# Optimization experiments

Hardware: AMD Instinct MI355X
Metric: run time of the kernel (lower is better)

The kernel has to match this reference:

```python
import jax, jax.numpy as jnp
import numpy as np

B, L = 131072, 24  # batch size, number of links (= n_dofs, all revolute)


def _skew(v):
    # v: [L, 3] -> [L, 3, 3] cross-product matrices
    zeros = jnp.zeros_like(v[:, 0])
    return jnp.stack([
        jnp.stack([zeros, -v[:, 2], v[:, 1]], axis=-1),
        jnp.stack([v[:, 2], zeros, -v[:, 0]], axis=-1),
        jnp.stack([-v[:, 1], v[:, 0], zeros], axis=-1),
    ], axis=-2)


def setup_inputs() -> dict:
    key = jax.random.key(0)
    k1, k2, k3, k4 = jax.random.split(key, 4)
    q = jax.random.normal(k1, (B, L), dtype=jnp.float32)
    qd = jax.random.normal(k2, (B, L), dtype=jnp.float32)
    axes = jax.random.normal(k3, (L, 3), dtype=jnp.float32)   # joint axes (normalized in reference)
    t_fix = jax.random.normal(k4, (L, 3), dtype=jnp.float32)  # fixed parent->joint translations
    return {"q": q, "qd": qd, "axes": axes, "t_fix": t_fix}


def reference(q, qd, axes, t_fix):
    # Stateless forward kinematics for all links of a serial revolute chain.
    # joint_pose_i = Trans(t_fix_i) @ Rot(axis_i, q_i);  pose_i = pose_{i-1} @ joint_pose_i
    dtype = q.dtype
    a = axes / jnp.linalg.norm(axes, axis=-1, keepdims=True)  # [L,3]
    K = _skew(a)                                              # [L,3,3]
    KK = jnp.einsum('lij,ljk->lik', K, K)
    s = jnp.sin(q)[..., None, None]                           # [B,L,1,1]
    c = jnp.cos(q)[..., None, None]
    I3 = jnp.eye(3, dtype=dtype)
    # Rodrigues: per-joint rotation [B,L,3,3]
    R_joint = I3 + s * K[None] + (1.0 - c) * KK[None]

    def step(carry, x):
        Rp, tp = carry          # parent pose: [B,3,3], [B,3]
        Rj, tf = x              # joint rotation [B,3,3], fixed translation [3]
        tc = tp + jnp.einsum('bij,j->bi', Rp, tf)
        Rc = jnp.einsum('bij,bjk->bik', Rp, Rj)
        return (Rc, tc), (Rc, tc)

    R0 = jnp.broadcast_to(I3, (q.shape[0], 3, 3))
    t0 = jnp.zeros((q.shape[0], 3), dtype=dtype)
    Rj_seq = jnp.moveaxis(R_joint, 1, 0)                      # [L,B,3,3]
    _, (Rs, ts) = jax.lax.scan(step, (R0, t0), (Rj_seq, t_fix))
    Rs = jnp.moveaxis(Rs, 0, 1)                               # [B,L,3,3]
    ts = jnp.moveaxis(ts, 0, 1)                               # [B,L,3]
    top = jnp.concatenate([Rs, ts[..., None]], axis=-1)       # [B,L,3,4]
    bottom = jnp.broadcast_to(jnp.array([0., 0., 0., 1.], dtype=dtype),
                              top.shape[:-2] + (1, 4))
    return jnp.concatenate([top, bottom], axis=-2)            # [B,L,4,4]
```

## Files before the change

### kernel.cpp

```cpp
#include <hip/hip_runtime.h>


typedef float v4 __attribute__((ext_vector_type(4)));

constexpr int L = 24;
constexpr int EW = 384;
constexpr int EWP = 388;
constexpr int WAVE_WORDS = 16 * EWP;

__global__ __launch_bounds__(128) void fk_kernel(
    const float* __restrict__ q,
    const float* __restrict__ axes,
    const float* __restrict__ tfix,
    float* __restrict__ out,
    int nb)
{
    __shared__ float s_a[L * 3];
    __shared__ float s_t[L * 3];
    __shared__ float s_buf[2 * WAVE_WORDS];

    if (threadIdx.x < L) {
        const int l = threadIdx.x;
        float ax = axes[l * 3 + 0], ay = axes[l * 3 + 1], az = axes[l * 3 + 2];
        float inv = rsqrtf(ax * ax + ay * ay + az * az);
        s_a[l * 3 + 0] = ax * inv;
        s_a[l * 3 + 1] = ay * inv;
        s_a[l * 3 + 2] = az * inv;
        s_t[l * 3 + 0] = tfix[l * 3 + 0];
        s_t[l * 3 + 1] = tfix[l * 3 + 1];
        s_t[l * 3 + 2] = tfix[l * 3 + 2];
    }
    __syncthreads();

    const int tid  = threadIdx.x;
    const int wave = tid >> 6;
    const int lane = tid & 63;
    const int e    = lane >> 2;
    const int r    = lane & 3;

    const int wave_elem0 = blockIdx.x * 32 + wave * 16;
    const int b = wave_elem0 + e;

    float* wbuf = s_buf + wave * WAVE_WORDS;

    if (b < nb) {
        float qv[L];
        {
            const v4* q4 = (const v4*)(q + (size_t)b * L);
            #pragma unroll
            for (int i = 0; i < L / 4; ++i) {
                v4 v = q4[i];
                qv[4 * i + 0] = v.x;
                qv[4 * i + 1] = v.y;
                qv[4 * i + 2] = v.z;
                qv[4 * i + 3] = v.w;
            }
        }

        float Ra = (r == 0) ? 1.f : 0.f;
        float Rb = (r == 1) ? 1.f : 0.f;
        float Rc = (r == 2) ? 1.f : 0.f;
        float t  = (r == 3) ? 1.f : 0.f;

        v4* lrow = (v4*)(wbuf + e * EWP + r * 4);

        #pragma unroll
        for (int l = 0; l < L; ++l) {
            const float ax = s_a[l * 3 + 0], ay = s_a[l * 3 + 1], az = s_a[l * 3 + 2];
            const float fx = s_t[l * 3 + 0], fy = s_t[l * 3 + 1], fz = s_t[l * 3 + 2];

            float s, c;
            __sincosf(qv[l], &s, &c);
            const float omc = 1.0f - c;

            const float xy = omc * ax * ay;
            const float xz = omc * ax * az;
            const float yz = omc * ay * az;
            const float J00 = c + omc * ax * ax;
            const float J11 = c + omc * ay * ay;
            const float J22 = c + omc * az * az;
            const float J01 = xy - s * az, J10 = xy + s * az;
            const float J02 = xz + s * ay, J20 = xz - s * ay;
            const float J12 = yz - s * ax, J21 = yz + s * ax;

            t += Ra * fx + Rb * fy + Rc * fz;

            const float na  = Ra * J00 + Rb * J10 + Rc * J20;
            const float nb_ = Ra * J01 + Rb * J11 + Rc * J21;
            const float nc  = Ra * J02 + Rb * J12 + Rc * J22;
            Ra = na; Rb = nb_; Rc = nc;

            lrow[l * 4] = v4{Ra, Rb, Rc, t};
        }
    }
    __syncthreads();

    if (wave_elem0 < nb) {
        float* gbase = out + (size_t)wave_elem0 * EW;
        #pragma unroll
        for (int j = 0; j < 24; ++j) {
            const unsigned w = (unsigned)(j * 256 + lane * 4);
            const unsigned elem = w / EW;
            const unsigned rem  = w - elem * EW;
            v4 v = *(const v4*)(wbuf + elem * EWP + rem);
            __builtin_nontemporal_store(v, (v4*)(gbase + w));
        }
    }
}

extern "C" void kernel_launch(void* const* d_in, const int* in_sizes, int n_in,
                              void* d_out, int out_size, void* d_ws, size_t ws_size,
                              hipStream_t stream) {
    const float* q    = (const float*)d_in[0];
    const float* axes = (const float*)d_in[2];
    const float* tfix = (const float*)d_in[3];
    float* out = (float*)d_out;

    const int nb = in_sizes[0] / L;
    const long long nthreads = (long long)nb * 4;
    const int grid = (int)((nthreads + 127) / 128);
    fk_kernel<<<grid, 128, 0, stream>>>(q, axes, tfix, out, nb);
}
```

Baseline: 222.2 us.

## Store outputs directly from registers, dropping the LDS staging buffer

Removes the per-wave shared-memory staging and the second coalesced, nontemporal write phase. Each thread now writes its 16-byte row straight to global memory, with four adjacent lanes covering 64 contiguous bytes per link. Per-link products of the axis components are precomputed into shared memory and the math is rewritten with explicit FMAs. Blocks grow to 256 threads with a 4-blocks occupancy hint. The risk is that the direct stores are strided across elements, 384 floats apart between lane groups, which may hurt write coalescing compared with the staged, fully contiguous stores.

Result: faster. 214.0 us (-3.7%).

```diff
diff --git a/kernel.cpp b/kernel.cpp
--- a/kernel.cpp
+++ b/kernel.cpp
@@ -4,107 +4,82 @@
 typedef float v4 __attribute__((ext_vector_type(4)));
 
 constexpr int L = 24;
-constexpr int EW = 384;
-constexpr int EWP = 388;
-constexpr int WAVE_WORDS = 16 * EWP;
 
-__global__ __launch_bounds__(128) void fk_kernel(
+__global__ __launch_bounds__(256, 4) void fk_kernel(
     const float* __restrict__ q,
     const float* __restrict__ axes,
     const float* __restrict__ tfix,
     float* __restrict__ out,
     int nb)
 {
-    __shared__ float s_a[L * 3];
-    __shared__ float s_t[L * 3];
-    __shared__ float s_buf[2 * WAVE_WORDS];
+    __shared__ float s_lnk[L][12];
 
     if (threadIdx.x < L) {
         const int l = threadIdx.x;
         float ax = axes[l * 3 + 0], ay = axes[l * 3 + 1], az = axes[l * 3 + 2];
         float inv = rsqrtf(ax * ax + ay * ay + az * az);
-        s_a[l * 3 + 0] = ax * inv;
-        s_a[l * 3 + 1] = ay * inv;
-        s_a[l * 3 + 2] = az * inv;
-        s_t[l * 3 + 0] = tfix[l * 3 + 0];
-        s_t[l * 3 + 1] = tfix[l * 3 + 1];
-        s_t[l * 3 + 2] = tfix[l * 3 + 2];
+        ax *= inv; ay *= inv; az *= inv;
+        s_lnk[l][0] = ax;             s_lnk[l][1] = ay;             s_lnk[l][2] = az;
+        s_lnk[l][3] = tfix[l * 3 + 0]; s_lnk[l][4] = tfix[l * 3 + 1]; s_lnk[l][5] = tfix[l * 3 + 2];
+        s_lnk[l][6] = ax * ax;        s_lnk[l][7] = ay * ay;
+        s_lnk[l][8] = az * az;        s_lnk[l][9] = ax * ay;
+        s_lnk[l][10] = ax * az;       s_lnk[l][11] = ay * az;
     }
     __syncthreads();
 
-    const int tid  = threadIdx.x;
-    const int wave = tid >> 6;
-    const int lane = tid & 63;
-    const int e    = lane >> 2;
-    const int r    = lane & 3;
+    const int tid = blockIdx.x * 256 + threadIdx.x;
+    const int b = tid >> 2;
+    const int r = tid & 3;
+    if (b >= nb) return;
 
-    const int wave_elem0 = blockIdx.x * 32 + wave * 16;
-    const int b = wave_elem0 + e;
-
-    float* wbuf = s_buf + wave * WAVE_WORDS;
-
-    if (b < nb) {
-        float qv[L];
-        {
-            const v4* q4 = (const v4*)(q + (size_t)b * L);
-            #pragma unroll
-            for (int i = 0; i < L / 4; ++i) {
-                v4 v = q4[i];
-                qv[4 * i + 0] = v.x;
-                qv[4 * i + 1] = v.y;
-                qv[4 * i + 2] = v.z;
-                qv[4 * i + 3] = v.w;
-            }
-        }
-
-        float Ra = (r == 0) ? 1.f : 0.f;
-        float Rb = (r == 1) ? 1.f : 0.f;
-        float Rc = (r == 2) ? 1.f : 0.f;
-        float t  = (r == 3) ? 1.f : 0.f;
-
-        v4* lrow = (v4*)(wbuf + e * EWP + r * 4);
-
+    float qv[L];
+    {
+        const v4* q4 = (const v4*)(q + (size_t)b * L);
         #pragma unroll
-        for (int l = 0; l < L; ++l) {
-            const float ax = s_a[l * 3 + 0], ay = s_a[l * 3 + 1], az = s_a[l * 3 + 2];
-            const float fx = s_t[l * 3 + 0], fy = s_t[l * 3 + 1], fz = s_t[l * 3 + 2];
-
-            float s, c;
-            __sincosf(qv[l], &s, &c);
-            const float omc = 1.0f - c;
-
-            const float xy = omc * ax * ay;
-            const float xz = omc * ax * az;
-            const float yz = omc * ay * az;
-            const float J00 = c + omc * ax * ax;
-            const float J11 = c + omc * ay * ay;
-            const float J22 = c + omc * az * az;
-            const float J01 = xy - s * az, J10 = xy + s * az;
-            const float J02 = xz + s * ay, J20 = xz - s * ay;
-            const float J12 = yz - s * ax, J21 = yz + s * ax;
-
-            t += Ra * fx + Rb * fy + Rc * fz;
-
-            const float na  = Ra * J00 + Rb * J10 + Rc * J20;
-            const float nb_ = Ra * J01 + Rb * J11 + Rc * J21;
-            const float nc  = Ra * J02 + Rb * J12 + Rc * J22;
-            Ra = na; Rb = nb_; Rc = nc;
-
-            lrow[l * 4] = v4{Ra, Rb, Rc, t};
+        for (int i = 0; i < L / 4; ++i) {
+            v4 v = q4[i];
+            qv[4 * i + 0] = v.x;
+            qv[4 * i + 1] = v.y;
+            qv[4 * i + 2] = v.z;
+            qv[4 * i + 3] = v.w;
         }
     }
-    __syncthreads();
 
-    if (wave_elem0 < nb) {
-        float* gbase = out + (size_t)wave_elem0 * EW;
-        #pragma unroll
-        for (int j = 0; j < 24; ++j) {
-            const unsigned w = (unsigned)(j * 256 + lane * 4);
-            const unsigned elem = w / EW;
-            const unsigned rem  = w - elem * EW;
-            v4 v = *(const v4*)(wbuf + elem * EWP + rem);
-            __builtin_nontemporal_store(v, (v4*)(gbase + w));
-        }
+    float Ra = (r == 0) ? 1.f : 0.f;
+    float Rb = (r == 1) ? 1.f : 0.f;
+    float Rc = (r == 2) ? 1.f : 0.f;
+    float t  = (r == 3) ? 1.f : 0.f;
+
+    v4* orow = (v4*)out + (size_t)b * (4 * L) + r;
+
+    #pragma unroll
+    for (int l = 0; l < L; ++l) {
+        const float ax = s_lnk[l][0], ay = s_lnk[l][1], az = s_lnk[l][2];
+        const float fx = s_lnk[l][3], fy = s_lnk[l][4], fz = s_lnk[l][5];
+        const float xx = s_lnk[l][6], yy = s_lnk[l][7], zz = s_lnk[l][8];
+        const float xy = s_lnk[l][9], xz = s_lnk[l][10], yz = s_lnk[l][11];
+
+        float s, c;
+        __sincosf(qv[l], &s, &c);
+        const float omc = 1.0f - c;
+
+        const float J00 = fmaf(omc, xx, c);
+        const float J11 = fmaf(omc, yy, c);
+        const float J22 = fmaf(omc, zz, c);
+        const float oxy = omc * xy, oxz = omc * xz, oyz = omc * yz;
+        const float sx = s * ax, sy = s * ay, sz = s * az;
+        const float J01 = oxy - sz, J10 = oxy + sz;
+        const float J02 = oxz + sy, J20 = oxz - sy;
+        const float J12 = oyz - sx, J21 = oyz + sx;
+
+        t = fmaf(Ra, fx, fmaf(Rb, fy, fmaf(Rc, fz, t)));
+
+        const float na  = fmaf(Ra, J00, fmaf(Rb, J10, Rc * J20));
+        const float nb_ = fmaf(Ra, J01, fmaf(Rb, J11, Rc * J21));
+        const float nc  = fmaf(Ra, J02, fmaf(Rb, J12, Rc * J22));
+        Ra = na; Rb = nb_; Rc = nc;
+
+        orow[l * 4] = v4{Ra, Rb, Rc, t};
     }
 }
 
@@ -118,6 +93,6 @@
 
     const int nb = in_sizes[0] / L;
     const long long nthreads = (long long)nb * 4;
-    const int grid = (int)((nthreads + 127) / 128);
-    fk_kernel<<<grid, 128, 0, stream>>>(q, axes, tfix, out, nb);
+    const int grid = (int)((nthreads + 255) / 256);
+    fk_kernel<<<grid, 256, 0, stream>>>(q, axes, tfix, out, nb);
 }
```
